# Kernel tuning notes

Measured on AMD Instinct MI355X. Metric: run time of the kernel, lower is better.

The kernel has to match this reference:

```python
import jax, jax.numpy as jnp
import numpy as np

E, K = 8, 2          # n_experts, top-k
D, O = 768, 3072     # input_size, output_size
B, S = 4, 512        # batch, seq


def setup_inputs() -> dict:
    key = jax.random.key(0)
    k1, k2, k3, k4, k5 = jax.random.split(key, 5)
    x = jax.random.normal(k1, (B, S, D), jnp.float32)
    w_gate = jax.random.normal(k2, (D, E), jnp.float32) * 0.02
    expert_w = jax.random.normal(k3, (E, O, D), jnp.float32) * 0.02
    expert_b = jax.random.normal(k4, (E, O), jnp.float32) * 0.02
    static_w = jax.random.normal(k5, (O, D), jnp.float32) * 0.02
    return {"x": x, "w_gate": w_gate, "expert_w": expert_w,
            "expert_b": expert_b, "static_w": static_w}


def cv_squared(v):
    # torch .var() is unbiased (ddof=1)
    return jnp.var(v, ddof=1) / (jnp.mean(v) ** 2 + 1e-10)


def reference(x, w_gate, expert_w, expert_b, static_w):
    loss_coef = 0.01
    xf = x.reshape(-1, D)                      # [N, D]
    N = xf.shape[0]

    # --- top-k gating (eval path: no noise) ---
    logits = xf @ w_gate                       # [N, E]
    top_v, top_i = jax.lax.top_k(logits, K + 1)
    top_k_gates = jax.nn.softmax(top_v[:, :K], axis=1)   # [N, K]
    gates = jnp.zeros_like(logits).at[
        jnp.arange(N)[:, None], top_i[:, :K]].set(top_k_gates)  # [N, E]

    importance = gates.sum(0)                  # [E]
    load = (gates > 0).sum(0).astype(jnp.float32)
    loss = (cv_squared(importance) + cv_squared(load)) * loss_coef

    # --- experts: F.linear(h, W_e + static_w, b_e), combined by gates ---
    W = expert_w + static_w[None]              # [E, O, D]
    y_e = jnp.einsum('nd,eod->neo', xf, W) + expert_b[None]   # [N, E, O]
    y = jnp.einsum('neo,ne->no', y_e, gates)   # [N, O]

    return y.reshape(B, S, O), loss
```

## Files before the change

kernel.cpp:

```cpp
#include <hip/hip_runtime.h>
#include <hip/hip_bf16.h>
#include <stdint.h>

#define E_ 8
#define D_ 768
#define O_ 3072
#define N_ 2048

typedef __attribute__((ext_vector_type(8))) __bf16 bf16x8;
typedef __attribute__((ext_vector_type(4))) float f32x4;

__device__ __forceinline__ unsigned short f2bf(float f) {
    union { float f; uint32_t u; } a; a.f = f;
    uint32_t u = a.u;
    uint32_t r = (u + 0x7fffu + ((u >> 16) & 1u)) >> 16;
    return (unsigned short)r;
}
__device__ __forceinline__ float bflo(uint32_t u) {
    union { uint32_t u; float f; } a; a.u = u << 16; return a.f;
}
__device__ __forceinline__ float bfhi(uint32_t u) {
    union { uint32_t u; float f; } a; a.u = u & 0xffff0000u; return a.f;
}

__device__ __forceinline__ void async16(const void* g, void* l) {
    __builtin_amdgcn_global_load_lds(
        (const __attribute__((address_space(1))) void*)g,
        (__attribute__((address_space(3))) void*)l, 16, 0, 0);
}

__global__ __launch_bounds__(256) void prologue_kernel(
    const float* __restrict__ x, const float* __restrict__ w_gate,
    const float* __restrict__ ew, const float* __restrict__ sw,
    unsigned short* __restrict__ xb, unsigned short* __restrict__ wb,
    int* __restrict__ choice_e, float* __restrict__ choice_g)
{
    if (blockIdx.x >= 512) {
        int i = (blockIdx.x - 512) * 256 + threadIdx.x;
        int f = i * 8;
        const int od = O_ * D_;
        int e = f / od;
        int rem = f - e * od;
        float4 a0 = *(const float4*)(ew + f);
        float4 a1 = *(const float4*)(ew + f + 4);
        float4 b0 = *(const float4*)(sw + rem);
        float4 b1 = *(const float4*)(sw + rem + 4);
        union { ushort u[8]; uint4 v; } o;
        o.u[0] = f2bf(a0.x + b0.x); o.u[1] = f2bf(a0.y + b0.y);
        o.u[2] = f2bf(a0.z + b0.z); o.u[3] = f2bf(a0.w + b0.w);
        o.u[4] = f2bf(a1.x + b1.x); o.u[5] = f2bf(a1.y + b1.y);
        o.u[6] = f2bf(a1.z + b1.z); o.u[7] = f2bf(a1.w + b1.w);
        ((uint4*)wb)[i] = o.v;
        return;
    }

    int wid  = threadIdx.x >> 6;
    int lane = threadIdx.x & 63;
    int n = blockIdx.x * 4 + wid;
    const float* xr = x + (size_t)n * D_;

    float acc[E_];
#pragma unroll
    for (int e = 0; e < E_; ++e) acc[e] = 0.f;

    for (int c = 0; c < D_ / 64; ++c) {
        int d = c * 64 + lane;
        float xv = xr[d];
        xb[(size_t)n * D_ + d] = f2bf(xv);
        const float* wg = w_gate + (size_t)d * E_;
        float4 w0 = *(const float4*)(wg);
        float4 w1 = *(const float4*)(wg + 4);
        acc[0] += xv * w0.x; acc[1] += xv * w0.y;
        acc[2] += xv * w0.z; acc[3] += xv * w0.w;
        acc[4] += xv * w1.x; acc[5] += xv * w1.y;
        acc[6] += xv * w1.z; acc[7] += xv * w1.w;
    }
#pragma unroll
    for (int e = 0; e < E_; ++e) {
        float v = acc[e];
        for (int off = 32; off > 0; off >>= 1) v += __shfl_xor(v, off, 64);
        acc[e] = v;
    }
    if (lane == 0) {
        int i0 = 0; float v0 = acc[0];
#pragma unroll
        for (int e = 1; e < E_; ++e) if (acc[e] > v0) { v0 = acc[e]; i0 = e; }
        int i1 = -1; float v1 = -3.0e38f;
#pragma unroll
        for (int e = 0; e < E_; ++e) if (e != i0 && acc[e] > v1) { v1 = acc[e]; i1 = e; }
        float ex = expf(v1 - v0);
        float g0 = 1.f / (1.f + ex);
        float g1 = ex / (1.f + ex);
        choice_e[2 * n]     = i0;  choice_g[2 * n]     = g0;
        choice_e[2 * n + 1] = i1;  choice_g[2 * n + 1] = g1;
    }
}

__global__ __launch_bounds__(1024) void compact_kernel(
    const int* __restrict__ choice_e, const float* __restrict__ choice_g,
    int* __restrict__ counts, int* __restrict__ pair_id,
    float* __restrict__ pair_gate, float* __restrict__ out_loss)
{
    __shared__ int   s_cnt[E_];
    __shared__ float s_imp[E_];
    int t = threadIdx.x;
    int lane = t & 63;
    if (t < E_) s_cnt[t] = 0;
    __syncthreads();

#pragma unroll
    for (int it = 0; it < (2 * N_) / 1024; ++it) {
        int i = it * 1024 + t;
        int ce = choice_e[i];
        float gv = choice_g[i];
        unsigned long long mask[E_];
#pragma unroll
        for (int e = 0; e < E_; ++e) mask[e] = __ballot(ce == e);
        int b = 0;
        if (lane < E_) b = atomicAdd(&s_cnt[lane], __popcll(mask[lane]));
        int mybase = __shfl(b, ce, 64);
        unsigned long long mymask = mask[0];
#pragma unroll
        for (int e = 1; e < E_; ++e) if (ce == e) mymask = mask[e];
        int pos = mybase + __popcll(mymask & ((1ull << lane) - 1ull));
        pair_id[ce * N_ + pos]   = i;
        pair_gate[ce * N_ + pos] = gv;
    }
    __syncthreads();
    if (t < E_) counts[t] = s_cnt[t];

    if (t < 256) {
        int e = t >> 5, l = t & 31;
        int cnt = s_cnt[e];
        float p = 0.f;
        for (int i = l; i < cnt; i += 32) p += pair_gate[e * N_ + i];
#pragma unroll
        for (int off = 16; off > 0; off >>= 1) p += __shfl_down(p, off, 32);
        if (l == 0) s_imp[e] = p;
    }
    __syncthreads();
    if (t == 0) {
        float mi = 0.f, ml = 0.f, imp[E_], ld[E_];
#pragma unroll
        for (int i = 0; i < E_; ++i) {
            imp[i] = s_imp[i]; ld[i] = (float)s_cnt[i];
            mi += imp[i]; ml += ld[i];
        }
        mi /= (float)E_; ml /= (float)E_;
        float vi = 0.f, vl = 0.f;
#pragma unroll
        for (int i = 0; i < E_; ++i) {
            vi += (imp[i] - mi) * (imp[i] - mi);
            vl += (ld[i] - ml) * (ld[i] - ml);
        }
        vi /= (float)(E_ - 1); vl /= (float)(E_ - 1);
        *out_loss = 0.01f * (vi / (mi * mi + 1e-10f) + vl / (ml * ml + 1e-10f));
    }
}

#define BM 128
#define BN 128
#define BK 32

__global__ __launch_bounds__(256) void moe_gemm_kernel(
    const unsigned short* __restrict__ xb,
    const unsigned short* __restrict__ wb,
    const float* __restrict__ expert_b,
    const int* __restrict__ counts,
    const int* __restrict__ pair_id,
    const float* __restrict__ pair_gate,
    unsigned short* __restrict__ part)
{
    int bid = blockIdx.x;
    int e  = bid & 7;
    int j  = bid >> 3;
    int nt = j >> 4;
    int mt = j & 15;
    int cnt = counts[e];
    int m0 = mt * BM;
    if (m0 >= cnt) return;
    int n0 = nt * BN;

    __shared__ __align__(16) unsigned short sA[2][BM * BK];
    __shared__ __align__(16) unsigned short sB[2][BN * BK];

    int tid  = threadIdx.x;
    int lane = tid & 63;
    int wid  = tid >> 6;
    int wm = wid & 1, wn = wid >> 1;
    int l16 = lane & 15;
    int quad = lane >> 4;

    const unsigned short* gA[2];
    const unsigned short* gB[2];
#pragma unroll
    for (int s = 0; s < 2; ++s) {
        int c = tid + 256 * s;
        int row = c >> 2;
        int kg = (c & 3) ^ (row & 3);
        int ar = m0 + row; if (ar >= cnt) ar = cnt - 1;
        gA[s] = xb + (size_t)(pair_id[e * N_ + ar] >> 1) * D_ + kg * 8;
        gB[s] = wb + ((size_t)e * O_ + n0 + row) * D_ + kg * 8;
    }
    char* lA[2] = { (char*)sA[0] + wid * 1024, (char*)sA[1] + wid * 1024 };
    char* lB[2] = { (char*)sB[0] + wid * 1024, (char*)sB[1] + wid * 1024 };

    f32x4 acc[4][4];
#pragma unroll
    for (int a = 0; a < 4; ++a)
#pragma unroll
        for (int b = 0; b < 4; ++b) acc[a][b] = (f32x4){0.f, 0.f, 0.f, 0.f};

#pragma unroll
    for (int s = 0; s < 2; ++s) {
        async16(gA[s], lA[0] + s * 4096);
        async16(gB[s], lB[0] + s * 4096);
    }

    int kb = 0;
    for (int k0 = 0; k0 < D_; k0 += BK, kb ^= 1) {
        __syncthreads();
        int kn = k0 + BK;
        if (kn < D_) {
#pragma unroll
            for (int s = 0; s < 2; ++s) {
                async16(gA[s] + kn, lA[kb ^ 1] + s * 4096);
                async16(gB[s] + kn, lB[kb ^ 1] + s * 4096);
            }
        }
        bf16x8 af[4], bfr[4];
#pragma unroll
        for (int mi = 0; mi < 4; ++mi) {
            int row = wm * 64 + mi * 16 + l16;
            int ch  = row * 4 + (quad ^ (row & 3));
            af[mi] = *(const bf16x8*)&sA[kb][ch * 8];
        }
#pragma unroll
        for (int ni = 0; ni < 4; ++ni) {
            int row = wn * 64 + ni * 16 + l16;
            int ch  = row * 4 + (quad ^ (row & 3));
            bfr[ni] = *(const bf16x8*)&sB[kb][ch * 8];
        }
#pragma unroll
        for (int mi = 0; mi < 4; ++mi)
#pragma unroll
            for (int ni = 0; ni < 4; ++ni)
                acc[mi][ni] = __builtin_amdgcn_mfma_f32_16x16x32_bf16(
                    af[mi], bfr[ni], acc[mi][ni], 0, 0, 0);
    }

    float bias[4];
#pragma unroll
    for (int ni = 0; ni < 4; ++ni)
        bias[ni] = expert_b[e * O_ + n0 + wn * 64 + ni * 16 + l16];
#pragma unroll
    for (int mi = 0; mi < 4; ++mi) {
        int rb = m0 + wm * 64 + mi * 16 + quad * 4;
#pragma unroll
        for (int reg = 0; reg < 4; ++reg) {
            int r = rb + reg;
            if (r < cnt) {
                int pid    = pair_id[e * N_ + r];
                float gate = pair_gate[e * N_ + r];
#pragma unroll
                for (int ni = 0; ni < 4; ++ni) {
                    int o = n0 + wn * 64 + ni * 16 + l16;
                    part[(size_t)pid * O_ + o] =
                        f2bf(gate * (acc[mi][ni][reg] + bias[ni]));
                }
            }
        }
    }
}

__global__ __launch_bounds__(256) void reduce_kernel(
    const unsigned short* __restrict__ part, float* __restrict__ y)
{
    int i = blockIdx.x * 256 + threadIdx.x;
    int n = i / (O_ / 8);
    int c = (i - n * (O_ / 8)) * 8;
    const uint4 p0 = *(const uint4*)(part + (size_t)(2 * n) * O_ + c);
    const uint4 p1 = *(const uint4*)(part + (size_t)(2 * n + 1) * O_ + c);
    float4 o0, o1;
    o0.x = bflo(p0.x) + bflo(p1.x); o0.y = bfhi(p0.x) + bfhi(p1.x);
    o0.z = bflo(p0.y) + bflo(p1.y); o0.w = bfhi(p0.y) + bfhi(p1.y);
    o1.x = bflo(p0.z) + bflo(p1.z); o1.y = bfhi(p0.z) + bfhi(p1.z);
    o1.z = bflo(p0.w) + bflo(p1.w); o1.w = bfhi(p0.w) + bfhi(p1.w);
    float* yp = y + (size_t)n * O_ + c;
    *(float4*)(yp)     = o0;
    *(float4*)(yp + 4) = o1;
}

extern "C" void kernel_launch(void* const* d_in, const int* in_sizes, int n_in,
                              void* d_out, int out_size, void* d_ws, size_t ws_size,
                              hipStream_t stream) {
    const float* x        = (const float*)d_in[0];
    const float* w_gate   = (const float*)d_in[1];
    const float* expert_w = (const float*)d_in[2];
    const float* expert_b = (const float*)d_in[3];
    const float* static_w = (const float*)d_in[4];
    float* out = (float*)d_out;

    char* ws = (char*)d_ws;
    int*   counts    = (int*)(ws + 0);
    int*   pair_id   = (int*)(ws + 4096);
    float* pair_gate = (float*)(ws + 69632);
    int*   choice_e  = (int*)(ws + 135168);
    float* choice_g  = (float*)(ws + 151552);
    unsigned short* xb   = (unsigned short*)(ws + 167936);
    unsigned short* wb   = (unsigned short*)(ws + 3313664);
    unsigned short* part = (unsigned short*)(ws + 41062400);

    prologue_kernel<<<512 + (E_ * O_ * D_ / 8) / 256, 256, 0, stream>>>(
        x, w_gate, expert_w, static_w, xb, wb, choice_e, choice_g);
    compact_kernel<<<1, 1024, 0, stream>>>(choice_e, choice_g, counts,
                                           pair_id, pair_gate, out + (size_t)N_ * O_);

    moe_gemm_kernel<<<E_ * 24 * 16, 256, 0, stream>>>(xb, wb, expert_b, counts,
                                                      pair_id, pair_gate, part);

    reduce_kernel<<<(N_ * O_ / 8) / 256, 256, 0, stream>>>(part, out);
}
```

Before: 205.4 us.

## Split MoE GEMM along K into two halves and sum partials in reduce

After: 203.0 us. No clear change (-1.2%).

```diff
diff --git a/kernel.cpp b/kernel.cpp
--- a/kernel.cpp
+++ b/kernel.cpp
@@ -161,6 +161,7 @@
 #define BM 128
 #define BN 128
 #define BK 32
+#define KH 384
 
 __global__ __launch_bounds__(256) void moe_gemm_kernel(
     const unsigned short* __restrict__ xb,
@@ -171,11 +172,10 @@
     const float* __restrict__ pair_gate,
     unsigned short* __restrict__ part)
 {
-    int bid = blockIdx.x;
-    int e  = bid & 7;
-    int j  = bid >> 3;
-    int nt = j >> 4;
-    int mt = j & 15;
+    int e  = blockIdx.z;
+    int mt = blockIdx.y;
+    int nt = blockIdx.x >> 1;
+    int kh = blockIdx.x & 1;
     int cnt = counts[e];
     int m0 = mt * BM;
     if (m0 >= cnt) return;
@@ -197,10 +197,10 @@
     for (int s = 0; s < 2; ++s) {
         int c = tid + 256 * s;
         int row = c >> 2;
-        int kg = (c & 3) ^ (row & 3);
+        int kg = (c & 3) ^ ((row >> 1) & 3);
         int ar = m0 + row; if (ar >= cnt) ar = cnt - 1;
-        gA[s] = xb + (size_t)(pair_id[e * N_ + ar] >> 1) * D_ + kg * 8;
-        gB[s] = wb + ((size_t)e * O_ + n0 + row) * D_ + kg * 8;
+        gA[s] = xb + (size_t)(pair_id[e * N_ + ar] >> 1) * D_ + kh * KH + kg * 8;
+        gB[s] = wb + ((size_t)e * O_ + n0 + row) * D_ + kh * KH + kg * 8;
     }
     char* lA[2] = { (char*)sA[0] + wid * 1024, (char*)sA[1] + wid * 1024 };
     char* lB[2] = { (char*)sB[0] + wid * 1024, (char*)sB[1] + wid * 1024 };
@@ -218,10 +218,10 @@
     }
 
     int kb = 0;
-    for (int k0 = 0; k0 < D_; k0 += BK, kb ^= 1) {
+    for (int k0 = 0; k0 < KH; k0 += BK, kb ^= 1) {
         __syncthreads();
         int kn = k0 + BK;
-        if (kn < D_) {
+        if (kn < KH) {
 #pragma unroll
             for (int s = 0; s < 2; ++s) {
                 async16(gA[s] + kn, lA[kb ^ 1] + s * 4096);
@@ -232,13 +232,13 @@
 #pragma unroll
         for (int mi = 0; mi < 4; ++mi) {
             int row = wm * 64 + mi * 16 + l16;
-            int ch  = row * 4 + (quad ^ (row & 3));
+            int ch  = row * 4 + (quad ^ ((row >> 1) & 3));
             af[mi] = *(const bf16x8*)&sA[kb][ch * 8];
         }
 #pragma unroll
         for (int ni = 0; ni < 4; ++ni) {
             int row = wn * 64 + ni * 16 + l16;
-            int ch  = row * 4 + (quad ^ (row & 3));
+            int ch  = row * 4 + (quad ^ ((row >> 1) & 3));
             bfr[ni] = *(const bf16x8*)&sB[kb][ch * 8];
         }
 #pragma unroll
@@ -252,7 +252,8 @@
     float bias[4];
 #pragma unroll
     for (int ni = 0; ni < 4; ++ni)
-        bias[ni] = expert_b[e * O_ + n0 + wn * 64 + ni * 16 + l16];
+        bias[ni] = kh ? 0.f : expert_b[e * O_ + n0 + wn * 64 + ni * 16 + l16];
+    unsigned short* pp = part + (size_t)kh * (2 * N_) * O_;
 #pragma unroll
     for (int mi = 0; mi < 4; ++mi) {
         int rb = m0 + wm * 64 + mi * 16 + quad * 4;
@@ -265,7 +266,7 @@
 #pragma unroll
                 for (int ni = 0; ni < 4; ++ni) {
                     int o = n0 + wn * 64 + ni * 16 + l16;
-                    part[(size_t)pid * O_ + o] =
+                    pp[(size_t)pid * O_ + o] =
                         f2bf(gate * (acc[mi][ni][reg] + bias[ni]));
                 }
             }
@@ -276,16 +277,23 @@
 __global__ __launch_bounds__(256) void reduce_kernel(
     const unsigned short* __restrict__ part, float* __restrict__ y)
 {
+    const size_t PH = (size_t)(2 * N_) * O_;
     int i = blockIdx.x * 256 + threadIdx.x;
     int n = i / (O_ / 8);
     int c = (i - n * (O_ / 8)) * 8;
-    const uint4 p0 = *(const uint4*)(part + (size_t)(2 * n) * O_ + c);
-    const uint4 p1 = *(const uint4*)(part + (size_t)(2 * n + 1) * O_ + c);
+    const uint4 a0 = *(const uint4*)(part + (size_t)(2 * n) * O_ + c);
+    const uint4 a1 = *(const uint4*)(part + (size_t)(2 * n + 1) * O_ + c);
+    const uint4 b0 = *(const uint4*)(part + PH + (size_t)(2 * n) * O_ + c);
+    const uint4 b1 = *(const uint4*)(part + PH + (size_t)(2 * n + 1) * O_ + c);
     float4 o0, o1;
-    o0.x = bflo(p0.x) + bflo(p1.x); o0.y = bfhi(p0.x) + bfhi(p1.x);
-    o0.z = bflo(p0.y) + bflo(p1.y); o0.w = bfhi(p0.y) + bfhi(p1.y);
-    o1.x = bflo(p0.z) + bflo(p1.z); o1.y = bfhi(p0.z) + bfhi(p1.z);
-    o1.z = bflo(p0.w) + bflo(p1.w); o1.w = bfhi(p0.w) + bfhi(p1.w);
+    o0.x = bflo(a0.x) + bflo(a1.x) + bflo(b0.x) + bflo(b1.x);
+    o0.y = bfhi(a0.x) + bfhi(a1.x) + bfhi(b0.x) + bfhi(b1.x);
+    o0.z = bflo(a0.y) + bflo(a1.y) + bflo(b0.y) + bflo(b1.y);
+    o0.w = bfhi(a0.y) + bfhi(a1.y) + bfhi(b0.y) + bfhi(b1.y);
+    o1.x = bflo(a0.z) + bflo(a1.z) + bflo(b0.z) + bflo(b1.z);
+    o1.y = bfhi(a0.z) + bfhi(a1.z) + bfhi(b0.z) + bfhi(b1.z);
+    o1.z = bflo(a0.w) + bflo(a1.w) + bflo(b0.w) + bflo(b1.w);
+    o1.w = bfhi(a0.w) + bfhi(a1.w) + bfhi(b0.w) + bfhi(b1.w);
     float* yp = y + (size_t)n * O_ + c;
     *(float4*)(yp)     = o0;
     *(float4*)(yp + 4) = o1;
@@ -316,8 +324,9 @@
     compact_kernel<<<1, 1024, 0, stream>>>(choice_e, choice_g, counts,
                                            pair_id, pair_gate, out + (size_t)N_ * O_);
 
-    moe_gemm_kernel<<<E_ * 24 * 16, 256, 0, stream>>>(xb, wb, expert_b, counts,
-                                                      pair_id, pair_gate, part);
+    dim3 grid(2 * (O_ / BN), N_ / BM, E_);
+    moe_gemm_kernel<<<grid, 256, 0, stream>>>(xb, wb, expert_b, counts,
+                                              pair_id, pair_gate, part);
 
     reduce_kernel<<<(N_ * O_ / 8) / 256, 256, 0, stream>>>(part, out);
 }
```
